# Optimization experiments

Measured on AMD Instinct MI355X. Metric: run time of the kernel, lower is better.

The kernel has to match this reference:

```python
import jax, jax.numpy as jnp
import numpy as np

B, S, E, NW = 16, 4096, 512, 8  # batch, seq, embed_dim, n_wires (=d_k)
H = E // NW  # num_heads = 64


def setup_inputs() -> dict:
    key = jax.random.key(0)
    ks = jax.random.split(key, 10)
    s = 1.0 / np.sqrt(E)
    return {
        "x": jax.random.normal(ks[0], (B, S, E), dtype=jnp.float32),
        "Wq": jax.random.normal(ks[1], (E, E), dtype=jnp.float32) * s,
        "bq": jnp.zeros((E,), dtype=jnp.float32),
        "Wk": jax.random.normal(ks[2], (E, E), dtype=jnp.float32) * s,
        "bk": jnp.zeros((E,), dtype=jnp.float32),
        "Wv": jax.random.normal(ks[3], (E, E), dtype=jnp.float32) * s,
        "bv": jnp.zeros((E,), dtype=jnp.float32),
        "Wo": jax.random.normal(ks[4], (E, E), dtype=jnp.float32) * s,
        "bo": jnp.zeros((E,), dtype=jnp.float32),
        "theta": jax.random.normal(ks[5], (NW,), dtype=jnp.float32) * 0.1,
    }


def reference(x, Wq, bq, Wk, bk, Wv, bv, Wo, bo, theta):
    b, s, e = x.shape
    h, dk = H, NW

    def qproj(t):
        # Quantum circuit on product state: RX(t_i) then RX(theta_i) on wire i,
        # measure PauliZ -> <Z_i> = cos(t_i + theta_i). Shape [B,S,H,NW].
        return jnp.cos(t.reshape(b, s, h, dk) + theta)

    q = qproj(x @ Wq.T + bq)
    k = qproj(x @ Wk.T + bk)
    v = qproj(x @ Wv.T + bv)

    # Faithful to original: tensors enter attention as [B, S, H, dk], so the
    # softmax attention is computed ACROSS HEADS for each token position.
    scale = 1.0 / np.sqrt(dk)
    scores = jnp.einsum("bsid,bsjd->bsij", q, k) * scale  # [B,S,H,H]
    p = jax.nn.softmax(scores, axis=-1)
    out = jnp.einsum("bsij,bsjd->bsid", p, v)  # [B,S,H,dk]

    # out.transpose(1,2).contiguous().view(B,-1,E) from the torch code
    out = jnp.transpose(out, (0, 2, 1, 3)).reshape(b, -1, e)
    return out @ Wo.T + bo
```

## Files before the change

### kernel.cpp

```cpp
#include <hip/hip_runtime.h>
#include <hip/hip_bf16.h>
#include <math.h>


typedef __attribute__((ext_vector_type(8))) short short8;
typedef __attribute__((ext_vector_type(4))) float floatx4;
typedef __attribute__((ext_vector_type(4))) int intx4;

static __device__ __forceinline__ unsigned short f2bf(float f) {
  unsigned u = __float_as_uint(f);
  u += 0x7fffu + ((u >> 16) & 1u);
  return (unsigned short)(u >> 16);
}
static __device__ __forceinline__ float bf2f(unsigned short h) {
  return __uint_as_float(((unsigned)h) << 16);
}

__global__ void cvt_kernel(const float* __restrict__ in, unsigned short* __restrict__ out, int n) {
  int i0 = (blockIdx.x * blockDim.x + threadIdx.x) * 4;
  int stride = gridDim.x * blockDim.x * 4;
  for (int i = i0; i < n; i += stride) {
    const float4 v = *reinterpret_cast<const float4*>(in + i);
    ushort4 o;
    o.x = f2bf(v.x); o.y = f2bf(v.y); o.z = f2bf(v.z); o.w = f2bf(v.w);
    *reinterpret_cast<ushort4*>(out + i) = o;
  }
}

template<int MODE>
__global__ __launch_bounds__(256) void gemm_kernel(
    const unsigned short* __restrict__ A,
    const unsigned short* __restrict__ W,
    const float* __restrict__ bias,
    const float* __restrict__ theta,
    unsigned short* __restrict__ outB,
    float* __restrict__ outF)
{
  __shared__ unsigned short As[128][72];
  __shared__ unsigned short Bs[128][72];

  const int tid = threadIdx.x;
  const int bid = blockIdx.x;
  const int m0 = (bid >> 2) << 7;
  const int n0 = (bid & 3) << 7;

  const int lane = tid & 63;
  const int w = tid >> 6;
  const int wm = (w >> 1) << 6;
  const int wn = (w & 1) << 6;
  const int lr = lane & 15;
  const int kg = lane >> 4;

  floatx4 acc[4][4] = {};

  for (int k0 = 0; k0 < 512; k0 += 64) {
    #pragma unroll
    for (int it = 0; it < 4; ++it) {
      int chunk = tid + it * 256;
      int row = chunk >> 3;
      int col = (chunk & 7) << 3;
      *reinterpret_cast<intx4*>(&As[row][col]) =
          *reinterpret_cast<const intx4*>(&A[(size_t)(m0 + row) * 512 + k0 + col]);
      *reinterpret_cast<intx4*>(&Bs[row][col]) =
          *reinterpret_cast<const intx4*>(&W[(size_t)(n0 + row) * 512 + k0 + col]);
    }
    __syncthreads();

    #pragma unroll
    for (int kk = 0; kk < 64; kk += 32) {
      short8 af[4], bfr[4];
      #pragma unroll
      for (int mi = 0; mi < 4; ++mi)
        af[mi] = *reinterpret_cast<const short8*>(&As[wm + mi * 16 + lr][kk + kg * 8]);
      #pragma unroll
      for (int ni = 0; ni < 4; ++ni)
        bfr[ni] = *reinterpret_cast<const short8*>(&Bs[wn + ni * 16 + lr][kk + kg * 8]);
      #pragma unroll
      for (int mi = 0; mi < 4; ++mi)
        #pragma unroll
        for (int ni = 0; ni < 4; ++ni)
          acc[mi][ni] = __builtin_amdgcn_mfma_f32_16x16x32_bf16(af[mi], bfr[ni], acc[mi][ni], 0, 0, 0);
    }
    __syncthreads();
  }

  float bl[4];
  #pragma unroll
  for (int ni = 0; ni < 4; ++ni) bl[ni] = bias[n0 + wn + ni * 16 + lr];
  float thl = 0.0f;
  if constexpr (MODE == 0) thl = theta[lr & 7];

  #pragma unroll
  for (int mi = 0; mi < 4; ++mi) {
    #pragma unroll
    for (int ni = 0; ni < 4; ++ni) {
      #pragma unroll
      for (int i = 0; i < 4; ++i) {
        int gm = m0 + wm + mi * 16 + kg * 4 + i;
        int gn = n0 + wn + ni * 16 + lr;
        float val = acc[mi][ni][i] + bl[ni];
        if constexpr (MODE == 0) {
          outB[(size_t)gm * 512 + gn] = f2bf(cosf(val + thl));
        } else {
          outF[(size_t)gm * 512 + gn] = val;
        }
      }
    }
  }
}

__global__ __launch_bounds__(256) void attn_kernel(
    const unsigned short* __restrict__ q,
    const unsigned short* __restrict__ k,
    const unsigned short* __restrict__ v,
    unsigned short* __restrict__ out)
{
  __shared__ float kf[4][64][9];
  __shared__ float vf[4][64][9];
  const int w = threadIdx.x >> 6;
  const int lane = threadIdx.x & 63;
  const int t = blockIdx.x * 4 + w;

  const size_t base = (size_t)t * 512 + lane * 8;
  short8 q8 = *reinterpret_cast<const short8*>(q + base);
  short8 k8 = *reinterpret_cast<const short8*>(k + base);
  short8 v8 = *reinterpret_cast<const short8*>(v + base);

  float qf[8];
  #pragma unroll
  for (int d = 0; d < 8; ++d) {
    qf[d] = bf2f((unsigned short)q8[d]);
    kf[w][lane][d] = bf2f((unsigned short)k8[d]);
    vf[w][lane][d] = bf2f((unsigned short)v8[d]);
  }
  __syncthreads();

  float s[64];
  #pragma unroll
  for (int j = 0; j < 64; ++j) {
    float a = 0.f;
    #pragma unroll
    for (int d = 0; d < 8; ++d) a += qf[d] * kf[w][j][d];
    s[j] = a;
  }
  float m = s[0];
  #pragma unroll
  for (int j = 1; j < 64; ++j) m = fmaxf(m, s[j]);

  const float c = 0.35355339059327f * 1.44269504089f;
  float o[8] = {0, 0, 0, 0, 0, 0, 0, 0};
  float sum = 0.f;
  #pragma unroll
  for (int j = 0; j < 64; ++j) {
    float p = exp2f((s[j] - m) * c);
    sum += p;
    #pragma unroll
    for (int d = 0; d < 8; ++d) o[d] += p * vf[w][j][d];
  }
  const float inv = 1.0f / sum;

  const int b = t >> 12;
  const int sidx = t & 4095;
  const int sb = sidx >> 6, si = sidx & 63;
  const size_t row = (size_t)(b << 12) + (lane << 6) + sb;
  short8 o8;
  #pragma unroll
  for (int d = 0; d < 8; ++d) o8[d] = (short)f2bf(o[d] * inv);
  *reinterpret_cast<short8*>(out + row * 512 + si * 8) = o8;
}

extern "C" void kernel_launch(void* const* d_in, const int* in_sizes, int n_in,
                              void* d_out, int out_size, void* d_ws, size_t ws_size,
                              hipStream_t stream) {
  const float* x     = (const float*)d_in[0];
  const float* Wq    = (const float*)d_in[1];
  const float* bq    = (const float*)d_in[2];
  const float* Wk    = (const float*)d_in[3];
  const float* bk    = (const float*)d_in[4];
  const float* Wv    = (const float*)d_in[5];
  const float* bv    = (const float*)d_in[6];
  const float* Wo    = (const float*)d_in[7];
  const float* bo    = (const float*)d_in[8];
  const float* theta = (const float*)d_in[9];
  float* out = (float*)d_out;

  char* ws = (char*)d_ws;
  const size_t MB = 1024ull * 1024ull;
  unsigned short* xb  = (unsigned short*)(ws);
  unsigned short* qb  = (unsigned short*)(ws + 64 * MB);
  unsigned short* kb  = (unsigned short*)(ws + 128 * MB);
  unsigned short* vb  = (unsigned short*)(ws + 192 * MB);
  unsigned short* wqb = (unsigned short*)(ws + 256 * MB);
  unsigned short* wkb = (unsigned short*)(ws + 256 * MB + 512 * 1024);
  unsigned short* wvb = (unsigned short*)(ws + 257 * MB);
  unsigned short* wob = (unsigned short*)(ws + 257 * MB + 512 * 1024);

  const int NX = 65536 * 512;
  const int NW2 = 512 * 512;

  cvt_kernel<<<2048, 256, 0, stream>>>(x, xb, NX);
  cvt_kernel<<<256, 256, 0, stream>>>(Wq, wqb, NW2);
  cvt_kernel<<<256, 256, 0, stream>>>(Wk, wkb, NW2);
  cvt_kernel<<<256, 256, 0, stream>>>(Wv, wvb, NW2);
  cvt_kernel<<<256, 256, 0, stream>>>(Wo, wob, NW2);

  gemm_kernel<0><<<2048, 256, 0, stream>>>(xb, wqb, bq, theta, qb, nullptr);
  gemm_kernel<0><<<2048, 256, 0, stream>>>(xb, wkb, bk, theta, kb, nullptr);
  gemm_kernel<0><<<2048, 256, 0, stream>>>(xb, wvb, bv, theta, vb, nullptr);

  attn_kernel<<<16384, 256, 0, stream>>>(qb, kb, vb, xb);

  gemm_kernel<1><<<2048, 256, 0, stream>>>(xb, wob, bo, nullptr, nullptr, out);
}
```

Baseline: 2.163 ms.

## Merge QKV projections into one launch and stage tiles with global_load_lds

The three Q/K/V projection GEMMs become a single launch of 6144 blocks, where each block picks its weight matrix, bias and output slice from its block index. Tile loads into shared memory now use the direct global-to-LDS load builtin instead of going through registers. The shared-memory tiles drop their 72-element padding, which may add LDS bank conflicts on the MFMA fragment reads. Launch bounds now ask for one block per SIMD, and the change aims to cut launch overhead, register staging and tail effects.

```diff
diff --git a/kernel.cpp b/kernel.cpp
--- a/kernel.cpp
+++ b/kernel.cpp
@@ -5,7 +5,6 @@
 
 typedef __attribute__((ext_vector_type(8))) short short8;
 typedef __attribute__((ext_vector_type(4))) float floatx4;
-typedef __attribute__((ext_vector_type(4))) int intx4;
 
 static __device__ __forceinline__ unsigned short f2bf(float f) {
   unsigned u = __float_as_uint(f);
@@ -14,6 +13,12 @@
 }
 static __device__ __forceinline__ float bf2f(unsigned short h) {
   return __uint_as_float(((unsigned)h) << 16);
+}
+
+static __device__ __forceinline__ void gload16(const void* g, void* l) {
+  __builtin_amdgcn_global_load_lds(
+      (const __attribute__((address_space(1))) void*)g,
+      (__attribute__((address_space(3))) void*)l, 16, 0, 0);
 }
 
 __global__ void cvt_kernel(const float* __restrict__ in, unsigned short* __restrict__ out, int n) {
@@ -27,22 +32,37 @@
   }
 }
 
-template<int MODE>
-__global__ __launch_bounds__(256) void gemm_kernel(
+template<int MODE, int NBLK>
+__global__ __launch_bounds__(256, 1) void gemm_kernel(
     const unsigned short* __restrict__ A,
-    const unsigned short* __restrict__ W,
-    const float* __restrict__ bias,
+    const unsigned short* __restrict__ W0,
+    const float* __restrict__ b0,
+    const float* __restrict__ b1,
+    const float* __restrict__ b2,
     const float* __restrict__ theta,
-    unsigned short* __restrict__ outB,
+    unsigned short* __restrict__ o0,
     float* __restrict__ outF)
 {
-  __shared__ unsigned short As[128][72];
-  __shared__ unsigned short Bs[128][72];
+  __shared__ unsigned short As[128 * 64];
+  __shared__ unsigned short Bs[128 * 64];
 
   const int tid = threadIdx.x;
   const int bid = blockIdx.x;
-  const int m0 = (bid >> 2) << 7;
-  const int n0 = (bid & 3) << 7;
+  const int m_blk = bid / NBLK;
+  const int n_blk = bid - m_blk * NBLK;
+  const int m0 = m_blk << 7;
+
+  const unsigned short* W;
+  const float* bias;
+  int n0, wsel = 0;
+  if constexpr (MODE == 0) {
+    wsel = n_blk >> 2;
+    n0 = (n_blk & 3) << 7;
+    W = W0 + (size_t)wsel * 262144;
+    bias = (wsel == 0) ? b0 : ((wsel == 1) ? b1 : b2);
+  } else {
+    W = W0; bias = b0; n0 = n_blk << 7;
+  }
 
   const int lane = tid & 63;
   const int w = tid >> 6;
@@ -51,18 +71,18 @@
   const int lr = lane & 15;
   const int kg = lane >> 4;
 
+  const int srow = lane >> 3;
+  const int scol = (lane & 7) << 3;
+
   floatx4 acc[4][4] = {};
 
   for (int k0 = 0; k0 < 512; k0 += 64) {
     #pragma unroll
-    for (int it = 0; it < 4; ++it) {
-      int chunk = tid + it * 256;
-      int row = chunk >> 3;
-      int col = (chunk & 7) << 3;
-      *reinterpret_cast<intx4*>(&As[row][col]) =
-          *reinterpret_cast<const intx4*>(&A[(size_t)(m0 + row) * 512 + k0 + col]);
-      *reinterpret_cast<intx4*>(&Bs[row][col]) =
-          *reinterpret_cast<const intx4*>(&W[(size_t)(n0 + row) * 512 + k0 + col]);
+    for (int i = 0; i < 4; ++i) {
+      const int chunk = (i << 2) | w;
+      const int row = (chunk << 3) + srow;
+      gload16(&A[(size_t)(m0 + row) * 512 + k0 + scol], &As[chunk << 9]);
+      gload16(&W[(size_t)(n0 + row) * 512 + k0 + scol], &Bs[chunk << 9]);
     }
     __syncthreads();
 
@@ -71,10 +91,10 @@
       short8 af[4], bfr[4];
       #pragma unroll
       for (int mi = 0; mi < 4; ++mi)
-        af[mi] = *reinterpret_cast<const short8*>(&As[wm + mi * 16 + lr][kk + kg * 8]);
+        af[mi] = *reinterpret_cast<const short8*>(&As[(wm + mi * 16 + lr) * 64 + kk + kg * 8]);
       #pragma unroll
       for (int ni = 0; ni < 4; ++ni)
-        bfr[ni] = *reinterpret_cast<const short8*>(&Bs[wn + ni * 16 + lr][kk + kg * 8]);
+        bfr[ni] = *reinterpret_cast<const short8*>(&Bs[(wn + ni * 16 + lr) * 64 + kk + kg * 8]);
       #pragma unroll
       for (int mi = 0; mi < 4; ++mi)
         #pragma unroll
@@ -100,7 +120,7 @@
         int gn = n0 + wn + ni * 16 + lr;
         float val = acc[mi][ni][i] + bl[ni];
         if constexpr (MODE == 0) {
-          outB[(size_t)gm * 512 + gn] = f2bf(cosf(val + thl));
+          o0[(size_t)wsel * 33554432 + (size_t)gm * 512 + gn] = f2bf(cosf(val + thl));
         } else {
           outF[(size_t)gm * 512 + gn] = val;
         }
@@ -188,12 +208,10 @@
   const size_t MB = 1024ull * 1024ull;
   unsigned short* xb  = (unsigned short*)(ws);
   unsigned short* qb  = (unsigned short*)(ws + 64 * MB);
-  unsigned short* kb  = (unsigned short*)(ws + 128 * MB);
-  unsigned short* vb  = (unsigned short*)(ws + 192 * MB);
   unsigned short* wqb = (unsigned short*)(ws + 256 * MB);
-  unsigned short* wkb = (unsigned short*)(ws + 256 * MB + 512 * 1024);
-  unsigned short* wvb = (unsigned short*)(ws + 257 * MB);
-  unsigned short* wob = (unsigned short*)(ws + 257 * MB + 512 * 1024);
+  unsigned short* wkb = wqb + 262144;
+  unsigned short* wvb = wqb + 524288;
+  unsigned short* wob = wqb + 786432;
 
   const int NX = 65536 * 512;
   const int NW2 = 512 * 512;
@@ -204,11 +222,9 @@
   cvt_kernel<<<256, 256, 0, stream>>>(Wv, wvb, NW2);
   cvt_kernel<<<256, 256, 0, stream>>>(Wo, wob, NW2);
 
-  gemm_kernel<0><<<2048, 256, 0, stream>>>(xb, wqb, bq, theta, qb, nullptr);
-  gemm_kernel<0><<<2048, 256, 0, stream>>>(xb, wkb, bk, theta, kb, nullptr);
-  gemm_kernel<0><<<2048, 256, 0, stream>>>(xb, wvb, bv, theta, vb, nullptr);
-
-  attn_kernel<<<16384, 256, 0, stream>>>(qb, kb, vb, xb);
-
-  gemm_kernel<1><<<2048, 256, 0, stream>>>(xb, wob, bo, nullptr, nullptr, out);
-}
+  gemm_kernel<0, 12><<<6144, 256, 0, stream>>>(xb, wqb, bq, bk, bv, theta, qb, nullptr);
+
+  attn_kernel<<<16384, 256, 0, stream>>>(qb, qb + 33554432, qb + 67108864, xb);
+
+  gemm_kernel<1, 4><<<2048, 256, 0, stream>>>(xb, wob, bo, nullptr, nullptr, nullptr, nullptr, out);
+}
```

New measurement: 2.019 ms. 6.6% less time.
